# Optimization experiments

Hardware: AMD Instinct MI355X
Metric: run time of the kernel (lower is better)

## Reference

```python
import jax, jax.numpy as jnp
import numpy as np

DIM = 768
HEADS = 8
HIDDEN = 3072
B, Hs, Ws = 16, 32, 32
N = Hs * Ws
LN_EPS = 1e-5


def setup_inputs() -> dict:
    key = jax.random.key(0)
    ks = jax.random.split(key, 10)
    s = lambda *sh: 0.02
    return {
        "x": jax.random.normal(ks[0], (B, N, DIM), jnp.float32),
        "Wq": jax.random.normal(ks[1], (DIM, DIM), jnp.float32) * 0.02,
        "temperature": jnp.ones((HEADS, 1, 1), jnp.float32),
        "fc1_w": jax.random.normal(ks[2], (HIDDEN, DIM), jnp.float32) * 0.02,
        "fc1_b": jnp.zeros((HIDDEN,), jnp.float32),
        "dw_w": jax.random.normal(ks[3], (HIDDEN, 1, 3, 3), jnp.float32) * 0.1,
        "dw_b": jnp.zeros((HIDDEN,), jnp.float32),
        "gamma": jnp.ones((HIDDEN,), jnp.float32),
        "fc2_w": jax.random.normal(ks[4], (DIM, HIDDEN), jnp.float32) * 0.02,
        "fc2_b": jnp.zeros((DIM,), jnp.float32),
        "ln_w": jnp.ones((DIM,), jnp.float32),
        "ln_b": jnp.zeros((DIM,), jnp.float32),
        "H": Hs,
        "W": Ws,
    }


def _dwconv(x, w, b, H, W):
    # x: (B, N, hidden) -> depthwise 3x3, pad 1 -> (B, N, hidden)
    Bn, Nn, Ch = x.shape
    img = x.transpose(0, 2, 1).reshape(Bn, Ch, H, W)
    out = jax.lax.conv_general_dilated(
        img, w, window_strides=(1, 1), padding=((1, 1), (1, 1)),
        dimension_numbers=("NCHW", "OIHW", "NCHW"), feature_group_count=Ch)
    out = out + b[None, :, None, None]
    return out.reshape(Bn, Ch, Nn).transpose(0, 2, 1)


def _layernorm(x, w, b):
    mu = x.mean(-1, keepdims=True)
    var = ((x - mu) ** 2).mean(-1, keepdims=True)
    return (x - mu) * jax.lax.rsqrt(var + LN_EPS) * w + b


def reference(x, Wq, temperature, fc1_w, fc1_b, dw_w, dw_b, gamma,
              fc2_w, fc2_b, ln_w, ln_b, H, W):
    # gpd_ratio == active_ratio == 1 -> pre/post scalings cancel
    Bn, Nn, C = x.shape
    h = temperature.shape[0]
    Ch = C // h
    # q/k/v heads: (B, h, N, Ch)
    q = (x @ Wq.T).reshape(Bn, Nn, h, Ch).transpose(0, 2, 1, 3)
    kv = x.reshape(Bn, Nn, h, Ch).transpose(0, 2, 1, 3)
    # channel attention: softmax over N, pool k over Ch, sigmoid gate
    qs = jax.nn.softmax(q, axis=-2).transpose(0, 1, 3, 2)      # (B,h,Ch,N)
    kp = jax.nn.softmax(kv, axis=-2).mean(-1, keepdims=True)    # (B,h,N,1)
    attn = jax.nn.sigmoid(qs @ kp) * temperature                # (B,h,Ch,1)
    # MLP on v (== x after scaling cancels): fc1 -> dwconv residual -> fc2 -> LN
    h1 = x @ fc1_w.T + fc1_b                                    # (B,N,hidden)
    h2 = gamma * _dwconv(h1, dw_w, dw_b, H, W) + h1
    v = _layernorm(h2 @ fc2_w.T + fc2_b, ln_w, ln_b)            # (B,N,C)
    v = v.reshape(Bn, Nn, h, Ch).transpose(0, 2, 1, 3)          # (B,h,N,Ch)
    prod = attn * v.transpose(0, 1, 3, 2)                       # (B,h,Ch,N)
    out = prod.transpose(0, 3, 1, 2).reshape(Bn, Nn, C)
    return out, prod.transpose(0, 1, 3, 2)
```

## Files before the change

### kernel.cpp

```cpp
#include <hip/hip_runtime.h>

#define BATCH 16
#define SEQ   1024
#define DIM   768
#define NHEAD 8
#define CHD   96
#define HID   3072
#define MTOT  (BATCH * SEQ)

using u16 = unsigned short;
typedef __attribute__((ext_vector_type(8))) short bf16x8;
typedef __attribute__((ext_vector_type(4))) float f32x4;

#define AS1 __attribute__((address_space(1)))
#define AS3 __attribute__((address_space(3)))

__device__ inline float bf2f(u16 u) {
    union { unsigned int i; float f; } v; v.i = ((unsigned int)u) << 16; return v.f;
}
__device__ inline u16 f2bf(float f) {
    union { float f; unsigned int i; } v; v.f = f;
    unsigned int r = v.i + 0x7FFFu + ((v.i >> 16) & 1u);
    return (u16)(r >> 16);
}

__device__ inline void gld16(const void* g, void* l) {
    __builtin_amdgcn_global_load_lds((AS1 const void*)g, (AS3 void*)l, 16, 0, 0);
}

template <bool HAS_BIAS>
__global__ __launch_bounds__(512, 2) void gemm256(const u16* __restrict__ A,
                                                  const u16* __restrict__ B,
                                                  const float* __restrict__ bias,
                                                  u16* __restrict__ C,
                                                  int M, int N, int K) {
    __shared__ u16 lds[4][2][256 * 32];
    const int tid = threadIdx.x;
    const int lane = tid & 63;
    const int wid = tid >> 6;
    const int wm = (wid >> 2) << 7;
    const int wn = (wid & 3) << 6;

    const int nwg = gridDim.x;
    const int wg = blockIdx.x;
    const int lid = (wg & 7) * (nwg >> 3) + (wg >> 3);
    const int nbx = N >> 8;
    const int mb = lid / nbx, nb = lid - mb * nbx;
    const int m0 = mb << 8, n0 = nb << 8;

    const int srow = tid >> 2;
    const int scol = (((tid & 3) << 4) ^ ((srow & 3) << 4)) >> 1;
    const u16* pa0 = A + (size_t)(m0 + srow) * K + scol;
    const u16* pa1 = A + (size_t)(m0 + 128 + srow) * K + scol;
    const u16* pb0 = B + (size_t)(n0 + srow) * K + scol;
    const u16* pb1 = B + (size_t)(n0 + 128 + srow) * K + scol;

    const int lrow = lane & 15;
    const int swcol = ((((lane >> 4) << 4) ^ ((lrow & 3) << 4)) >> 1);

    f32x4 acc[8][4] = {};

#define STAGE256(bf, kk) do {                                   \
    gld16(pa0 + (kk), &lds[bf][0][tid * 8]);                    \
    gld16(pa1 + (kk), &lds[bf][0][(512 + tid) * 8]);            \
    gld16(pb0 + (kk), &lds[bf][1][tid * 8]);                    \
    gld16(pb1 + (kk), &lds[bf][1][(512 + tid) * 8]);            \
} while (0)

    const int NT = K >> 5;
    STAGE256(0, 0);
    STAGE256(1, 32);
    STAGE256(2, 64);

    for (int T = 0; T < NT; ++T) {
        const int rem = NT - 1 - T;
        if (rem >= 2)      asm volatile("s_waitcnt vmcnt(8)" ::: "memory");
        else if (rem == 1) asm volatile("s_waitcnt vmcnt(4)" ::: "memory");
        else               asm volatile("s_waitcnt vmcnt(0)" ::: "memory");
        __builtin_amdgcn_sched_barrier(0);
        __builtin_amdgcn_s_barrier();
        __builtin_amdgcn_sched_barrier(0);

        const u16* Ab = lds[T & 3][0];
        const u16* Bb = lds[T & 3][1];

        bf16x8 bfr[4], afr[4];
#pragma unroll
        for (int j = 0; j < 4; ++j)
            bfr[j] = *(const bf16x8*)&Bb[(wn + j * 16 + lrow) * 32 + swcol];
#pragma unroll
        for (int i = 0; i < 4; ++i)
            afr[i] = *(const bf16x8*)&Ab[(wm + i * 16 + lrow) * 32 + swcol];

        if (T + 3 < NT) STAGE256((T + 3) & 3, (T + 3) * 32);

        asm volatile("s_waitcnt lgkmcnt(0)" ::: "memory");
        __builtin_amdgcn_sched_barrier(0);
        __builtin_amdgcn_s_setprio(1);
#pragma unroll
        for (int i = 0; i < 4; ++i)
#pragma unroll
            for (int j = 0; j < 4; ++j)
                acc[i][j] = __builtin_amdgcn_mfma_f32_16x16x32_bf16(afr[i], bfr[j], acc[i][j], 0, 0, 0);
        __builtin_amdgcn_s_setprio(0);

        bf16x8 afr2[4];
#pragma unroll
        for (int i = 0; i < 4; ++i)
            afr2[i] = *(const bf16x8*)&Ab[(wm + (i + 4) * 16 + lrow) * 32 + swcol];
        asm volatile("s_waitcnt lgkmcnt(0)" ::: "memory");
        __builtin_amdgcn_sched_barrier(0);
        __builtin_amdgcn_s_setprio(1);
#pragma unroll
        for (int i = 0; i < 4; ++i)
#pragma unroll
            for (int j = 0; j < 4; ++j)
                acc[i + 4][j] = __builtin_amdgcn_mfma_f32_16x16x32_bf16(afr2[i], bfr[j], acc[i + 4][j], 0, 0, 0);
        __builtin_amdgcn_s_setprio(0);
    }
#undef STAGE256

    const int crow = (lane >> 4) << 2, ccol = lane & 15;
#pragma unroll
    for (int i = 0; i < 8; ++i) {
        const int gm = m0 + wm + i * 16 + crow;
#pragma unroll
        for (int j = 0; j < 4; ++j) {
            const int gn = n0 + wn + j * 16 + ccol;
            const float bv = HAS_BIAS ? bias[gn] : 0.f;
#pragma unroll
            for (int r = 0; r < 4; ++r)
                C[(size_t)(gm + r) * N + gn] = f2bf(acc[i][j][r] + bv);
        }
    }
}

__global__ __launch_bounds__(256) void cvt_f2bf(const float* __restrict__ in,
                                                u16* __restrict__ out, int n4) {
    int i = blockIdx.x * 256 + threadIdx.x;
    if (i >= n4) return;
    float4 v = reinterpret_cast<const float4*>(in)[i];
    ushort4 o;
    o.x = f2bf(v.x); o.y = f2bf(v.y); o.z = f2bf(v.z); o.w = f2bf(v.w);
    reinterpret_cast<ushort4*>(out)[i] = o;
}

template <typename T>
__global__ __launch_bounds__(256) void colsm_stats(const T* __restrict__ X,
                                                   float* __restrict__ Mo,
                                                   float* __restrict__ So,
                                                   int ncols) {
    const int tid = threadIdx.x, lane = tid & 63, chunk = tid >> 6;
    const int b = blockIdx.y;
    const int j = blockIdx.x * 64 + lane;
    const T* p = X + (size_t)b * SEQ * ncols + j;
    float m = -3.0e38f, s = 0.f;
    const int nEnd = (chunk + 1) << 8;
    for (int n = chunk << 8; n < nEnd; ++n) {
        float raw;
        if constexpr (sizeof(T) == 2) raw = bf2f(p[(size_t)n * ncols]);
        else raw = p[(size_t)n * ncols];
        float nm = fmaxf(m, raw);
        s = s * __expf(m - nm) + __expf(raw - nm);
        m = nm;
    }
    __shared__ float ms[4][64], ss[4][64];
    ms[chunk][lane] = m; ss[chunk][lane] = s;
    __syncthreads();
    if (tid < 64) {
        float M = fmaxf(fmaxf(ms[0][lane], ms[1][lane]), fmaxf(ms[2][lane], ms[3][lane]));
        float S = ss[0][lane] * __expf(ms[0][lane] - M) + ss[1][lane] * __expf(ms[1][lane] - M) +
                  ss[2][lane] * __expf(ms[2][lane] - M) + ss[3][lane] * __expf(ms[3][lane] - M);
        Mo[b * ncols + j] = M;
        So[b * ncols + j] = S;
    }
}

__global__ __launch_bounds__(256) void kp_k(const float* __restrict__ x,
                                            const float* __restrict__ Mx,
                                            const float* __restrict__ Sx,
                                            float* __restrict__ kp) {
    const int n = blockIdx.x, b = blockIdx.y, tid = threadIdx.x;
    __shared__ float p[DIM];
    const float* row = x + ((size_t)b * SEQ + n) * DIM;
#pragma unroll
    for (int q = 0; q < 3; ++q) {
        int j = tid + (q << 8);
        p[j] = __expf(row[j] - Mx[b * DIM + j]) / Sx[b * DIM + j];
    }
    __syncthreads();
    if (tid < NHEAD) {
        float s = 0.f;
        for (int c = 0; c < CHD; ++c) s += p[tid * CHD + c];
        kp[((size_t)b * NHEAD + tid) * SEQ + n] = s * (1.f / (float)CHD);
    }
}

__global__ __launch_bounds__(256) void attn_k(const u16* __restrict__ Q,
                                              const float* __restrict__ Mq,
                                              const float* __restrict__ Sq,
                                              const float* __restrict__ kp,
                                              const float* __restrict__ temp,
                                              float* __restrict__ attnv) {
    const int tid = threadIdx.x, lane = tid & 63, chunk = tid >> 6;
    const int b = blockIdx.y;
    const int j = blockIdx.x * 64 + lane;
    const int h = j / CHD;
    const float mq = Mq[b * DIM + j];
    const u16* qp = Q + (size_t)b * SEQ * DIM + j;
    const float* kpp = kp + ((size_t)b * NHEAD + h) * SEQ;
    float acc = 0.f;
    const int nEnd = (chunk + 1) << 8;
    for (int n = chunk << 8; n < nEnd; ++n)
        acc += __expf(bf2f(qp[(size_t)n * DIM]) - mq) * kpp[n];
    __shared__ float accs[4][64];
    accs[chunk][lane] = acc;
    __syncthreads();
    if (tid < 64) {
        float a = accs[0][lane] + accs[1][lane] + accs[2][lane] + accs[3][lane];
        float z = a / Sq[b * DIM + j];
        attnv[b * DIM + j] = temp[h] / (1.f + __expf(-z));
    }
}

__global__ __launch_bounds__(128) void dwconv_v(const u16* __restrict__ h1,
                                                const float* __restrict__ w,
                                                const float* __restrict__ dwb,
                                                const float* __restrict__ gamma,
                                                u16* __restrict__ h2) {
    const int g = blockIdx.x * 128 + threadIdx.x;
    const int y = blockIdx.y >> 2;
    const int xw0 = (blockIdx.y & 3) << 3;
    const int b = blockIdx.z;
    const int ch0 = g << 3;

    float wreg[8][9], bias2[8];
#pragma unroll
    for (int c = 0; c < 8; ++c) {
        const float gm = gamma[ch0 + c];
#pragma unroll
        for (int k = 0; k < 9; ++k) wreg[c][k] = gm * w[(ch0 + c) * 9 + k];
        wreg[c][4] += 1.0f;
        bias2[c] = gm * dwb[ch0 + c];
    }

    float acc[8][8];
#pragma unroll
    for (int xo = 0; xo < 8; ++xo)
#pragma unroll
        for (int c = 0; c < 8; ++c) acc[xo][c] = bias2[c];

    const u16* base = h1 + (size_t)b * SEQ * HID + ch0;
#pragma unroll
    for (int dy = 0; dy < 3; ++dy) {
        const int yy = y + dy - 1;
        if ((unsigned)yy > 31u) continue;
#pragma unroll
        for (int cr = -1; cr <= 8; ++cr) {
            const int col = xw0 + cr;
            if ((unsigned)col > 31u) continue;
            const uint4 v = *reinterpret_cast<const uint4*>(
                base + (size_t)((yy << 5) + col) * HID);
            float f[8];
            f[0] = bf2f((u16)(v.x & 0xffff)); f[1] = bf2f((u16)(v.x >> 16));
            f[2] = bf2f((u16)(v.y & 0xffff)); f[3] = bf2f((u16)(v.y >> 16));
            f[4] = bf2f((u16)(v.z & 0xffff)); f[5] = bf2f((u16)(v.z >> 16));
            f[6] = bf2f((u16)(v.w & 0xffff)); f[7] = bf2f((u16)(v.w >> 16));
            const int xlo = cr > 0 ? cr - 1 : 0;
            const int xhi = cr < 7 ? cr + 1 : 7;
#pragma unroll
            for (int xo = 0; xo < 8; ++xo) {
                if (xo < xlo || xo > xhi) continue;
                const int dx = cr - xo + 1;
#pragma unroll
                for (int c = 0; c < 8; ++c)
                    acc[xo][c] += f[c] * wreg[c][dy * 3 + dx];
            }
        }
    }

#pragma unroll
    for (int xo = 0; xo < 8; ++xo) {
        const int n = (y << 5) + xw0 + xo;
        uint4 o;
        o.x = (unsigned)f2bf(acc[xo][0]) | ((unsigned)f2bf(acc[xo][1]) << 16);
        o.y = (unsigned)f2bf(acc[xo][2]) | ((unsigned)f2bf(acc[xo][3]) << 16);
        o.z = (unsigned)f2bf(acc[xo][4]) | ((unsigned)f2bf(acc[xo][5]) << 16);
        o.w = (unsigned)f2bf(acc[xo][6]) | ((unsigned)f2bf(acc[xo][7]) << 16);
        *reinterpret_cast<uint4*>(h2 + ((size_t)b * SEQ + n) * HID + ch0) = o;
    }
}

__global__ __launch_bounds__(256) void ln_out_k(const u16* __restrict__ vpre,
                                                const float* __restrict__ lnw,
                                                const float* __restrict__ lnb,
                                                const float* __restrict__ attnv,
                                                float* __restrict__ out,
                                                float* __restrict__ out2) {
    const int n = blockIdx.x, b = blockIdx.y, tid = threadIdx.x;
    __shared__ float red[4];
    const u16* row = vpre + ((size_t)b * SEQ + n) * DIM;
    float v[3];
    float s = 0.f;
#pragma unroll
    for (int q = 0; q < 3; ++q) { v[q] = bf2f(row[tid + (q << 8)]); s += v[q]; }
#pragma unroll
    for (int o = 32; o; o >>= 1) s += __shfl_down(s, o, 64);
    if ((tid & 63) == 0) red[tid >> 6] = s;
    __syncthreads();
    const float mu = (red[0] + red[1] + red[2] + red[3]) * (1.f / (float)DIM);
    __syncthreads();
    float vs = 0.f;
#pragma unroll
    for (int q = 0; q < 3; ++q) { float d = v[q] - mu; vs += d * d; }
#pragma unroll
    for (int o = 32; o; o >>= 1) vs += __shfl_down(vs, o, 64);
    if ((tid & 63) == 0) red[tid >> 6] = vs;
    __syncthreads();
    const float rstd = rsqrtf((red[0] + red[1] + red[2] + red[3]) * (1.f / (float)DIM) + 1e-5f);
    const float* at = attnv + b * DIM;
    float* orow = out + ((size_t)b * SEQ + n) * DIM;
#pragma unroll
    for (int q = 0; q < 3; ++q) {
        int j = tid + (q << 8);
        float o = (v[q] - mu) * rstd * lnw[j] + lnb[j];
        o *= at[j];
        orow[j] = o;
        int h = j / CHD, c = j - h * CHD;
        out2[(((size_t)b * NHEAD + h) * SEQ + n) * CHD + c] = o;
    }
}

extern "C" void kernel_launch(void* const* d_in, const int* in_sizes, int n_in,
                              void* d_out, int out_size, void* d_ws, size_t ws_size,
                              hipStream_t stream) {
    const float* x     = (const float*)d_in[0];
    const float* Wq    = (const float*)d_in[1];
    const float* temp  = (const float*)d_in[2];
    const float* fc1w  = (const float*)d_in[3];
    const float* fc1b  = (const float*)d_in[4];
    const float* dww   = (const float*)d_in[5];
    const float* dwb   = (const float*)d_in[6];
    const float* gamma = (const float*)d_in[7];
    const float* fc2w  = (const float*)d_in[8];
    const float* fc2b  = (const float*)d_in[9];
    const float* lnw   = (const float*)d_in[10];
    const float* lnb   = (const float*)d_in[11];

    float* out  = (float*)d_out;
    float* out2 = out + (size_t)BATCH * SEQ * DIM;

    char* ws = (char*)d_ws;
    u16* xb     = (u16*)ws;
    u16* h1     = (u16*)(ws + 25165824);
    u16* Wqb    = (u16*)(ws + 125829120);
    u16* fc1wb  = (u16*)(ws + 127008768);
    u16* fc2wb  = (u16*)(ws + 131727360);
    float* Mx   = (float*)(ws + 136445952);
    float* Sx   = Mx + BATCH * DIM;
    float* Mq   = Sx + BATCH * DIM;
    float* Sq   = Mq + BATCH * DIM;
    float* kp   = Sq + BATCH * DIM;
    float* attnv = kp + BATCH * NHEAD * SEQ;
    u16* vpreb  = xb;

    u16* Qb = (u16*)d_out;
    u16* h2 = (u16*)d_out;

    cvt_f2bf<<<(MTOT * DIM / 4 + 255) / 256, 256, 0, stream>>>(x, xb, MTOT * DIM / 4);
    cvt_f2bf<<<(DIM * DIM / 4 + 255) / 256, 256, 0, stream>>>(Wq, Wqb, DIM * DIM / 4);
    cvt_f2bf<<<(HID * DIM / 4 + 255) / 256, 256, 0, stream>>>(fc1w, fc1wb, HID * DIM / 4);
    cvt_f2bf<<<(DIM * HID / 4 + 255) / 256, 256, 0, stream>>>(fc2w, fc2wb, DIM * HID / 4);

    gemm256<false><<<(MTOT / 256) * (DIM / 256), 512, 0, stream>>>(
        xb, Wqb, nullptr, Qb, MTOT, DIM, DIM);
    colsm_stats<float><<<dim3(DIM / 64, BATCH), 256, 0, stream>>>(x, Mx, Sx, DIM);
    colsm_stats<u16><<<dim3(DIM / 64, BATCH), 256, 0, stream>>>(Qb, Mq, Sq, DIM);
    kp_k<<<dim3(SEQ, BATCH), 256, 0, stream>>>(x, Mx, Sx, kp);
    attn_k<<<dim3(DIM / 64, BATCH), 256, 0, stream>>>(Qb, Mq, Sq, kp, temp, attnv);

    gemm256<true><<<(MTOT / 256) * (HID / 256), 512, 0, stream>>>(
        xb, fc1wb, fc1b, h1, MTOT, HID, DIM);
    dwconv_v<<<dim3(3, 128, BATCH), 128, 0, stream>>>(h1, dww, dwb, gamma, h2);
    gemm256<true><<<(MTOT / 256) * (DIM / 256), 512, 0, stream>>>(
        h2, fc2wb, fc2b, vpreb, MTOT, DIM, HID);
    ln_out_k<<<dim3(SEQ, BATCH), 256, 0, stream>>>(vpreb, lnw, lnb, attnv, out, out2);
}
```

Measured before the change: 411.4 us.

## Restructure GEMM to double-buffered K=64 tiles with interleaved staging barriers

The bf16 GEMM used to run a 4-deep ring of K=32 LDS tiles. It now double-buffers K=64 tiles with an 8-way XOR swizzle. Each tile is processed in four MFMA phases separated by workgroup barriers, and the next tile's A and B global-to-LDS loads are issued inside the first two phases. This halves the number of loop iterations and is meant to overlap loads with compute in a ping-pong style. In exchange, prefetch depth drops to one tile, there are many more barriers per iteration, and each iteration ends with a full vmcnt(0) wait, which can expose memory latency.

Result: no change. 408.6 us (-0.7%).

```diff
diff --git a/kernel.cpp b/kernel.cpp
--- a/kernel.cpp
+++ b/kernel.cpp
@@ -34,7 +34,7 @@
                                                   const float* __restrict__ bias,
                                                   u16* __restrict__ C,
                                                   int M, int N, int K) {
-    __shared__ u16 lds[4][2][256 * 32];
+    __shared__ u16 lds[2][2][256 * 64];
     const int tid = threadIdx.x;
     const int lane = tid & 63;
     const int wid = tid >> 6;
@@ -48,52 +48,47 @@
     const int mb = lid / nbx, nb = lid - mb * nbx;
     const int m0 = mb << 8, n0 = nb << 8;
 
-    const int srow = tid >> 2;
-    const int scol = (((tid & 3) << 4) ^ ((srow & 3) << 4)) >> 1;
-    const u16* pa0 = A + (size_t)(m0 + srow) * K + scol;
-    const u16* pa1 = A + (size_t)(m0 + 128 + srow) * K + scol;
-    const u16* pb0 = B + (size_t)(n0 + srow) * K + scol;
-    const u16* pb1 = B + (size_t)(n0 + 128 + srow) * K + scol;
+    const int srow = tid >> 3;
+    const int sce = ((tid & 7) << 3) ^ ((srow & 7) << 3);
+    const u16* pa = A + (size_t)(m0 + srow) * K + sce;
+    const u16* pb = B + (size_t)(n0 + srow) * K + sce;
+    const size_t gstep = (size_t)64 * K;
+
+#define STAGE_OP(dst, p, kb) do {                               \
+    gld16((p) + (kb),             (dst) + tid * 8);             \
+    gld16((p) + (kb) + gstep,     (dst) + 4096 + tid * 8);      \
+    gld16((p) + (kb) + 2 * gstep, (dst) + 8192 + tid * 8);      \
+    gld16((p) + (kb) + 3 * gstep, (dst) + 12288 + tid * 8);     \
+} while (0)
 
     const int lrow = lane & 15;
-    const int swcol = ((((lane >> 4) << 4) ^ ((lrow & 3) << 4)) >> 1);
+    const int swz = (lrow & 7) << 4;
+    const int cb0 = (((lane >> 4) << 4) ^ swz) >> 1;
+    const int cb1 = ((64 | ((lane >> 4) << 4)) ^ swz) >> 1;
 
     f32x4 acc[8][4] = {};
 
-#define STAGE256(bf, kk) do {                                   \
-    gld16(pa0 + (kk), &lds[bf][0][tid * 8]);                    \
-    gld16(pa1 + (kk), &lds[bf][0][(512 + tid) * 8]);            \
-    gld16(pb0 + (kk), &lds[bf][1][tid * 8]);                    \
-    gld16(pb1 + (kk), &lds[bf][1][(512 + tid) * 8]);            \
-} while (0)
-
-    const int NT = K >> 5;
-    STAGE256(0, 0);
-    STAGE256(1, 32);
-    STAGE256(2, 64);
-
-    for (int T = 0; T < NT; ++T) {
-        const int rem = NT - 1 - T;
-        if (rem >= 2)      asm volatile("s_waitcnt vmcnt(8)" ::: "memory");
-        else if (rem == 1) asm volatile("s_waitcnt vmcnt(4)" ::: "memory");
-        else               asm volatile("s_waitcnt vmcnt(0)" ::: "memory");
-        __builtin_amdgcn_sched_barrier(0);
-        __builtin_amdgcn_s_barrier();
-        __builtin_amdgcn_sched_barrier(0);
-
-        const u16* Ab = lds[T & 3][0];
-        const u16* Bb = lds[T & 3][1];
-
-        bf16x8 bfr[4], afr[4];
-#pragma unroll
-        for (int j = 0; j < 4; ++j)
-            bfr[j] = *(const bf16x8*)&Bb[(wn + j * 16 + lrow) * 32 + swcol];
-#pragma unroll
-        for (int i = 0; i < 4; ++i)
-            afr[i] = *(const bf16x8*)&Ab[(wm + i * 16 + lrow) * 32 + swcol];
-
-        if (T + 3 < NT) STAGE256((T + 3) & 3, (T + 3) * 32);
-
+    const int NT = K >> 6;
+    STAGE_OP(&lds[0][0][0], pa, 0);
+    STAGE_OP(&lds[0][1][0], pb, 0);
+    asm volatile("s_waitcnt vmcnt(0)" ::: "memory");
+    __builtin_amdgcn_s_barrier();
+
+    for (int t = 0; t < NT; ++t) {
+        const u16* Ab = lds[t & 1][0];
+        const u16* Bb = lds[t & 1][1];
+        u16* An = &lds[(t + 1) & 1][0][0];
+        u16* Bn = &lds[(t + 1) & 1][1][0];
+        const size_t kb = (size_t)(t + 1) << 6;
+        const bool pre = (t + 1 < NT);
+
+        bf16x8 b0[4], b1[4], af[4];
+#pragma unroll
+        for (int j = 0; j < 4; ++j) b0[j] = *(const bf16x8*)&Bb[(wn + j * 16 + lrow) * 64 + cb0];
+#pragma unroll
+        for (int i = 0; i < 4; ++i) af[i] = *(const bf16x8*)&Ab[(wm + i * 16 + lrow) * 64 + cb0];
+        if (pre) STAGE_OP(An, pa, kb);
+        __builtin_amdgcn_s_barrier();
         asm volatile("s_waitcnt lgkmcnt(0)" ::: "memory");
         __builtin_amdgcn_sched_barrier(0);
         __builtin_amdgcn_s_setprio(1);
@@ -101,13 +96,14 @@
         for (int i = 0; i < 4; ++i)
 #pragma unroll
             for (int j = 0; j < 4; ++j)
-                acc[i][j] = __builtin_amdgcn_mfma_f32_16x16x32_bf16(afr[i], bfr[j], acc[i][j], 0, 0, 0);
+                acc[i][j] = __builtin_amdgcn_mfma_f32_16x16x32_bf16(af[i], b0[j], acc[i][j], 0, 0, 0);
         __builtin_amdgcn_s_setprio(0);
-
-        bf16x8 afr2[4];
-#pragma unroll
-        for (int i = 0; i < 4; ++i)
-            afr2[i] = *(const bf16x8*)&Ab[(wm + (i + 4) * 16 + lrow) * 32 + swcol];
+        __builtin_amdgcn_s_barrier();
+
+#pragma unroll
+        for (int i = 0; i < 4; ++i) af[i] = *(const bf16x8*)&Ab[(wm + 64 + i * 16 + lrow) * 64 + cb0];
+        if (pre) STAGE_OP(Bn, pb, kb);
+        __builtin_amdgcn_s_barrier();
         asm volatile("s_waitcnt lgkmcnt(0)" ::: "memory");
         __builtin_amdgcn_sched_barrier(0);
         __builtin_amdgcn_s_setprio(1);
@@ -115,10 +111,43 @@
         for (int i = 0; i < 4; ++i)
 #pragma unroll
             for (int j = 0; j < 4; ++j)
-                acc[i + 4][j] = __builtin_amdgcn_mfma_f32_16x16x32_bf16(afr2[i], bfr[j], acc[i + 4][j], 0, 0, 0);
+                acc[i + 4][j] = __builtin_amdgcn_mfma_f32_16x16x32_bf16(af[i], b0[j], acc[i + 4][j], 0, 0, 0);
         __builtin_amdgcn_s_setprio(0);
-    }
-#undef STAGE256
+        __builtin_amdgcn_s_barrier();
+
+#pragma unroll
+        for (int j = 0; j < 4; ++j) b1[j] = *(const bf16x8*)&Bb[(wn + j * 16 + lrow) * 64 + cb1];
+#pragma unroll
+        for (int i = 0; i < 4; ++i) af[i] = *(const bf16x8*)&Ab[(wm + i * 16 + lrow) * 64 + cb1];
+        __builtin_amdgcn_s_barrier();
+        asm volatile("s_waitcnt lgkmcnt(0)" ::: "memory");
+        __builtin_amdgcn_sched_barrier(0);
+        __builtin_amdgcn_s_setprio(1);
+#pragma unroll
+        for (int i = 0; i < 4; ++i)
+#pragma unroll
+            for (int j = 0; j < 4; ++j)
+                acc[i][j] = __builtin_amdgcn_mfma_f32_16x16x32_bf16(af[i], b1[j], acc[i][j], 0, 0, 0);
+        __builtin_amdgcn_s_setprio(0);
+        __builtin_amdgcn_s_barrier();
+
+#pragma unroll
+        for (int i = 0; i < 4; ++i) af[i] = *(const bf16x8*)&Ab[(wm + 64 + i * 16 + lrow) * 64 + cb1];
+        __builtin_amdgcn_s_barrier();
+        asm volatile("s_waitcnt lgkmcnt(0)" ::: "memory");
+        __builtin_amdgcn_sched_barrier(0);
+        __builtin_amdgcn_s_setprio(1);
+#pragma unroll
+        for (int i = 0; i < 4; ++i)
+#pragma unroll
+            for (int j = 0; j < 4; ++j)
+                acc[i + 4][j] = __builtin_amdgcn_mfma_f32_16x16x32_bf16(af[i], b1[j], acc[i + 4][j], 0, 0, 0);
+        __builtin_amdgcn_s_setprio(0);
+        asm volatile("s_waitcnt vmcnt(0)" ::: "memory");
+        __builtin_amdgcn_sched_barrier(0);
+        __builtin_amdgcn_s_barrier();
+    }
+#undef STAGE_OP
 
     const int crow = (lane >> 4) << 2, ccol = lane & 15;
 #pragma unroll
```
